# Optimization experiments

Measured on AMD Instinct MI355X. Metric: run time of the kernel, lower is better.

## Reference

```python
import jax, jax.numpy as jnp
import numpy as np

R = 8192        # rays
S_C = 64        # coarse samples per ray
S_F = 128       # fine samples per ray
NEAR, FAR = 2.0, 6.0
HIDDEN = 64
WHITE_BKGD = True
EPS_T = 1e-10   # transmittance eps (matches volumetric_rendering)
EPS_W = 1e-5    # weight-sum padding eps (matches piecewise_constant_pdf)


def setup_inputs() -> dict:
    key = jax.random.key(0)
    k0, k1, k2, k3, k4, k5 = jax.random.split(key, 6)
    return {
        "ray_origins": jax.random.normal(k0, (R, 3), jnp.float32),
        "ray_directions": jax.random.normal(k1, (R, 3), jnp.float32),
        "W1": jax.random.normal(k2, (6, HIDDEN), jnp.float32) * 0.5,
        "b1": jax.random.normal(k3, (HIDDEN,), jnp.float32) * 0.1,
        "W2": jax.random.normal(k4, (HIDDEN, 4), jnp.float32) * 0.3,
        "b2": jax.random.normal(k5, (4,), jnp.float32) * 0.1,
    }


def _mlp(coords, viewdirs, W1, b1, W2, b2):
    # coords: [R,S,3], viewdirs: [R,3] -> raw_rgb [R,S,3], raw_sigma [R,S]
    vd = jnp.broadcast_to(viewdirs[:, None, :], coords.shape)
    x = jnp.concatenate([coords, vd], axis=-1)            # [R,S,6]
    h = jax.nn.relu(jnp.einsum('rsi,ih->rsh', x, W1) + b1)
    out = jnp.einsum('rsh,ho->rso', h, W2) + b2           # [R,S,4]
    return out[..., :3], out[..., 3]


def _volrender(rgb, sigma, z_vals, directions):
    # rgb [R,S,3], sigma [R,S], z_vals [R,S], directions [R,3]
    dists = (z_vals[:, 1:] - z_vals[:, :-1]) * jnp.linalg.norm(directions, axis=-1, keepdims=True)
    alpha = 1.0 - jnp.exp(-sigma[:, :-1] * dists)         # [R,S-1]
    trans = jnp.concatenate([jnp.ones_like(alpha[:, :1]),
                             jnp.cumprod(1.0 - alpha + EPS_T, axis=-1)], axis=-1)
    alpha = jnp.concatenate([alpha, jnp.ones_like(alpha[:, :1])], axis=-1)
    weights = alpha * trans                               # [R,S]
    comp_rgb = jnp.einsum('rs,rsc->rc', weights, rgb)
    acc = weights.sum(-1)
    depth = (weights * z_vals).sum(-1)
    if WHITE_BKGD:
        comp_rgb = comp_rgb + (1.0 - acc)[:, None]
    return comp_rgb, weights, depth


def _piecewise_constant_pdf(bins, weights, num_samples):
    # bins [R,B+1], weights [R,B]; deterministic branch (randomized=False)
    nbins = weights.shape[-1]
    wsum = weights.sum(-1, keepdims=True)
    padding = jnp.maximum(0.0, EPS_W - wsum)
    weights = weights + padding / nbins
    wsum = wsum + padding
    pdf = weights / wsum
    cdf = jnp.minimum(1.0, jnp.cumsum(pdf[:, :-1], axis=-1))
    cdf = jnp.concatenate([jnp.zeros_like(cdf[:, :1]), cdf, jnp.ones_like(cdf[:, :1])], axis=-1)  # [R,B+1]
    u = jnp.linspace(0.0, 1.0 - jnp.finfo(jnp.float32).eps, num_samples)  # [F]
    mask = u[None, None, :] >= cdf[:, :, None]            # [R,B+1,F]

    def find_interval(x):  # x [R,B+1]
        x0 = jnp.max(jnp.where(mask, x[:, :, None], x[:, :1, None]), axis=1)
        x1 = jnp.min(jnp.where(~mask, x[:, :, None], x[:, -1:, None]), axis=1)
        return x0, x1

    bins_g0, bins_g1 = find_interval(bins)
    cdf_g0, cdf_g1 = find_interval(cdf)
    t = jnp.clip(jnp.nan_to_num((u[None, :] - cdf_g0) / (cdf_g1 - cdf_g0), nan=0.0), 0.0, 1.0)
    return jax.lax.stop_gradient(bins_g0 + t * (bins_g1 - bins_g0))  # [R,F]


def reference(ray_origins, ray_directions, W1, b1, W2, b2):
    Rn = ray_origins.shape[0]
    viewdirs = ray_directions / jnp.linalg.norm(ray_directions, axis=-1, keepdims=True)
    # coarse stratification (lindisp=False, randomized=False)
    t = jnp.linspace(0.0, 1.0, S_C)
    z_vals = jnp.broadcast_to(NEAR * (1.0 - t) + FAR * t, (Rn, S_C))
    coords = ray_origins[:, None, :] + z_vals[..., None] * ray_directions[:, None, :]
    raw_rgb, raw_sigma = _mlp(coords, viewdirs, W1, b1, W2, b2)
    rgb, sigma = jax.nn.sigmoid(raw_rgb), jax.nn.relu(raw_sigma)
    coarse_rgb, weights, coarse_depth = _volrender(rgb, sigma, z_vals, ray_directions)
    # hierarchical fine sampling via inverse-CDF over midpoint bins
    z_mid = 0.5 * (z_vals[:, 1:] + z_vals[:, :-1])
    z_samples = _piecewise_constant_pdf(z_mid, weights[:, 1:-1], S_F)
    z_fine = jnp.sort(jnp.concatenate([z_vals, z_samples], axis=-1), axis=-1)  # [R,S_C+S_F]
    coords = ray_origins[:, None, :] + z_fine[..., None] * ray_directions[:, None, :]
    # source falls through to coarse_model in the non-stateful branch; we mirror that (same MLP)
    raw_rgb, raw_sigma = _mlp(coords, viewdirs, W1, b1, W2, b2)
    rgb, sigma = jax.nn.sigmoid(raw_rgb), jax.nn.relu(raw_sigma)
    fine_rgb, _, fine_depth = _volrender(rgb, sigma, z_fine, ray_directions)
    return jnp.concatenate([coarse_rgb, coarse_depth[:, None], fine_rgb, fine_depth[:, None]], axis=-1)  # [R,8]
```

## Files before the change

kernel.cpp:

```cpp
#include <hip/hip_runtime.h>
#include <math.h>


#define RAYS   8192
#define NEARP  2.0f
#define FARP   6.0f
#define EPS_T  1e-10f
#define EPS_W  1e-5f
#define F32EPS 1.1920929e-7f

__device__ __forceinline__ float zc(int i) {
    const float t = (float)i * (1.0f / 63.0f);
    return NEARP * (1.0f - t) + FARP * t;
}
__device__ __forceinline__ float sigm(float x) { return 1.f / (1.f + __expf(-x)); }

__global__ __launch_bounds__(256) void nerf_kernel(
    const float* __restrict__ ro, const float* __restrict__ rd,
    const float* __restrict__ W1, const float* __restrict__ b1,
    const float* __restrict__ W2, const float* __restrict__ b2,
    float* __restrict__ out)
{
    __shared__ __align__(16) float sA[4][64];
    __shared__ __align__(16) float sB[4][64];
    __shared__ float sCdf[4][64];
    __shared__ float sZc [4][64];
    __shared__ float sZs [4][128];
    __shared__ float sZf [4][192];

    const int tid  = threadIdx.x;
    const int w    = tid >> 6;
    const int lane = tid & 63;
    const int ray  = blockIdx.x * 4 + w;

    const float ox = ro[ray * 3 + 0], oy = ro[ray * 3 + 1], oz = ro[ray * 3 + 2];
    const float dx = rd[ray * 3 + 0], dy = rd[ray * 3 + 1], dz = rd[ray * 3 + 2];
    const float norm = sqrtf(dx * dx + dy * dy + dz * dz);
    const float inv  = 1.f / norm;
    const float vx = dx * inv, vy = dy * inv, vz = dz * inv;

    {
        const float w10 = W1[lane],       w11 = W1[64 + lane],  w12 = W1[128 + lane];
        const float w13 = W1[192 + lane], w14 = W1[256 + lane], w15 = W1[320 + lane];
        float A = b1[lane];
        A = fmaf(vz, w15, A); A = fmaf(vy, w14, A); A = fmaf(vx, w13, A);
        A = fmaf(oz, w12, A); A = fmaf(oy, w11, A); A = fmaf(ox, w10, A);
        const float B = fmaf(dx, w10, fmaf(dy, w11, dz * w12));
        sA[w][lane] = A; sB[w][lane] = B;
    }
    __syncthreads();

    const float4* W2v = (const float4*)W2;
    const float bb0 = b2[0], bb1 = b2[1], bb2 = b2[2], bb3 = b2[3];

    const float z = zc(lane);
    sZc[w][lane] = z;
    float o0 = bb0, o1 = bb1, o2 = bb2, o3 = bb3;
#pragma unroll 4
    for (int i = 0; i < 16; ++i) {
        const float4 a4 = ((const float4*)sA[w])[i];
        const float4 b4 = ((const float4*)sB[w])[i];
        const float4 q0 = W2v[4 * i + 0], q1 = W2v[4 * i + 1];
        const float4 q2 = W2v[4 * i + 2], q3 = W2v[4 * i + 3];
        const float h0 = fmaxf(fmaf(z, b4.x, a4.x), 0.f);
        const float h1 = fmaxf(fmaf(z, b4.y, a4.y), 0.f);
        const float h2 = fmaxf(fmaf(z, b4.z, a4.z), 0.f);
        const float h3 = fmaxf(fmaf(z, b4.w, a4.w), 0.f);
        o0 = fmaf(h0, q0.x, o0); o1 = fmaf(h0, q0.y, o1); o2 = fmaf(h0, q0.z, o2); o3 = fmaf(h0, q0.w, o3);
        o0 = fmaf(h1, q1.x, o0); o1 = fmaf(h1, q1.y, o1); o2 = fmaf(h1, q1.z, o2); o3 = fmaf(h1, q1.w, o3);
        o0 = fmaf(h2, q2.x, o0); o1 = fmaf(h2, q2.y, o1); o2 = fmaf(h2, q2.z, o2); o3 = fmaf(h2, q2.w, o3);
        o0 = fmaf(h3, q3.x, o0); o1 = fmaf(h3, q3.y, o1); o2 = fmaf(h3, q3.z, o2); o3 = fmaf(h3, q3.w, o3);
    }
    const float r   = sigm(o0), g = sigm(o1), bl = sigm(o2);
    const float sig = fmaxf(o3, 0.f);

    const float znext = __shfl_down(z, 1);
    const float dist  = (znext - z) * norm;
    const float alpha = (lane < 63) ? (1.f - __expf(-sig * dist)) : 1.f;
    const float vfac  = 1.f - alpha + EPS_T;
    float p = vfac;
#pragma unroll
    for (int off = 1; off < 64; off <<= 1) {
        const float q = __shfl_up(p, off);
        if (lane >= off) p *= q;
    }
    float excl = __shfl_up(p, 1);
    if (lane == 0) excl = 1.f;
    const float wgt = alpha * excl;

    float sr = wgt * r, sg = wgt * g, sb = wgt * bl, sd = wgt * z;
#pragma unroll
    for (int m = 1; m < 64; m <<= 1) {
        sr += __shfl_xor(sr, m); sg += __shfl_xor(sg, m);
        sb += __shfl_xor(sb, m); sd += __shfl_xor(sd, m);
    }

    const float wmraw = __shfl_down(wgt, 1);
    const float wmv   = (lane < 62) ? wmraw : 0.f;
    float wsum = wmv;
#pragma unroll
    for (int m = 1; m < 64; m <<= 1) wsum += __shfl_xor(wsum, m);
    const float pad  = fmaxf(0.f, EPS_W - wsum);
    const float wadj = wmv + pad * (1.0f / 62.0f);
    const float wsp  = wsum + pad;
    const float pdf  = (lane < 62) ? (wadj / wsp) : 0.f;
    float ps = pdf;
#pragma unroll
    for (int off = 1; off < 64; off <<= 1) {
        const float q = __shfl_up(ps, off);
        if (lane >= off) ps += q;
    }
    if (lane < 61)  sCdf[w][lane + 1] = fminf(1.f, ps);
    if (lane == 61) sCdf[w][0]  = 0.f;
    if (lane == 62) sCdf[w][62] = 1.f;
    __syncthreads();

    float zsv[2];
#pragma unroll
    for (int j = 0; j < 2; ++j) {
        const int f = lane * 2 + j;
        const float u = (float)f * ((1.0f - F32EPS) / 127.0f);
        int lo = 0, hi = 62;
        while (hi - lo > 1) {
            const int mid = (lo + hi) >> 1;
            if (sCdf[w][mid] <= u) lo = mid; else hi = mid;
        }
        const float c0 = sCdf[w][lo], c1 = sCdf[w][lo + 1];
        const float den = c1 - c0;
        float tt = (den > 0.f) ? (u - c0) / den : 0.f;
        tt = fminf(fmaxf(tt, 0.f), 1.f);
        const float za = zc(lo), zb = zc(lo + 1), zd = zc(lo + 2);
        const float bin0 = 0.5f * (za + zb), bin1 = 0.5f * (zb + zd);
        const float zs = fmaf(tt, bin1 - bin0, bin0);
        zsv[j] = zs;
        sZs[w][f] = zs;
    }
    __syncthreads();

    {
        int lo = 0, hi = 128;
        while (lo < hi) { const int mid = (lo + hi) >> 1; if (sZs[w][mid] < z) lo = mid + 1; else hi = mid; }
        sZf[w][lane + lo] = z;
    }
#pragma unroll
    for (int j = 0; j < 2; ++j) {
        const float bv = zsv[j];
        const int f = lane * 2 + j;
        int lo = 0, hi = 64;
        while (lo < hi) { const int mid = (lo + hi) >> 1; if (sZc[w][mid] <= bv) lo = mid + 1; else hi = mid; }
        sZf[w][f + lo] = bv;
    }
    __syncthreads();

    const float zf0 = sZf[w][3 * lane + 0];
    const float zf1 = sZf[w][3 * lane + 1];
    const float zf2 = sZf[w][3 * lane + 2];
    const float zn2 = sZf[w][min(3 * lane + 3, 191)];

    float a0 = bb0, a1 = bb1, a2 = bb2, a3 = bb3;
    float e0 = bb0, e1 = bb1, e2 = bb2, e3 = bb3;
    float f0 = bb0, f1 = bb1, f2 = bb2, f3 = bb3;
#pragma unroll 2
    for (int i = 0; i < 16; ++i) {
        const float4 a4 = ((const float4*)sA[w])[i];
        const float4 b4 = ((const float4*)sB[w])[i];
        const float4 q0 = W2v[4 * i + 0], q1 = W2v[4 * i + 1];
        const float4 q2 = W2v[4 * i + 2], q3 = W2v[4 * i + 3];
        const float hA0 = fmaxf(fmaf(zf0, b4.x, a4.x), 0.f);
        const float hA1 = fmaxf(fmaf(zf0, b4.y, a4.y), 0.f);
        const float hA2 = fmaxf(fmaf(zf0, b4.z, a4.z), 0.f);
        const float hA3 = fmaxf(fmaf(zf0, b4.w, a4.w), 0.f);
        const float hB0 = fmaxf(fmaf(zf1, b4.x, a4.x), 0.f);
        const float hB1 = fmaxf(fmaf(zf1, b4.y, a4.y), 0.f);
        const float hB2 = fmaxf(fmaf(zf1, b4.z, a4.z), 0.f);
        const float hB3 = fmaxf(fmaf(zf1, b4.w, a4.w), 0.f);
        const float hC0 = fmaxf(fmaf(zf2, b4.x, a4.x), 0.f);
        const float hC1 = fmaxf(fmaf(zf2, b4.y, a4.y), 0.f);
        const float hC2 = fmaxf(fmaf(zf2, b4.z, a4.z), 0.f);
        const float hC3 = fmaxf(fmaf(zf2, b4.w, a4.w), 0.f);
        a0 = fmaf(hA0, q0.x, a0); a1 = fmaf(hA0, q0.y, a1); a2 = fmaf(hA0, q0.z, a2); a3 = fmaf(hA0, q0.w, a3);
        a0 = fmaf(hA1, q1.x, a0); a1 = fmaf(hA1, q1.y, a1); a2 = fmaf(hA1, q1.z, a2); a3 = fmaf(hA1, q1.w, a3);
        a0 = fmaf(hA2, q2.x, a0); a1 = fmaf(hA2, q2.y, a1); a2 = fmaf(hA2, q2.z, a2); a3 = fmaf(hA2, q2.w, a3);
        a0 = fmaf(hA3, q3.x, a0); a1 = fmaf(hA3, q3.y, a1); a2 = fmaf(hA3, q3.z, a2); a3 = fmaf(hA3, q3.w, a3);
        e0 = fmaf(hB0, q0.x, e0); e1 = fmaf(hB0, q0.y, e1); e2 = fmaf(hB0, q0.z, e2); e3 = fmaf(hB0, q0.w, e3);
        e0 = fmaf(hB1, q1.x, e0); e1 = fmaf(hB1, q1.y, e1); e2 = fmaf(hB1, q1.z, e2); e3 = fmaf(hB1, q1.w, e3);
        e0 = fmaf(hB2, q2.x, e0); e1 = fmaf(hB2, q2.y, e1); e2 = fmaf(hB2, q2.z, e2); e3 = fmaf(hB2, q2.w, e3);
        e0 = fmaf(hB3, q3.x, e0); e1 = fmaf(hB3, q3.y, e1); e2 = fmaf(hB3, q3.z, e2); e3 = fmaf(hB3, q3.w, e3);
        f0 = fmaf(hC0, q0.x, f0); f1 = fmaf(hC0, q0.y, f1); f2 = fmaf(hC0, q0.z, f2); f3 = fmaf(hC0, q0.w, f3);
        f0 = fmaf(hC1, q1.x, f0); f1 = fmaf(hC1, q1.y, f1); f2 = fmaf(hC1, q1.z, f2); f3 = fmaf(hC1, q1.w, f3);
        f0 = fmaf(hC2, q2.x, f0); f1 = fmaf(hC2, q2.y, f1); f2 = fmaf(hC2, q2.z, f2); f3 = fmaf(hC2, q2.w, f3);
        f0 = fmaf(hC3, q3.x, f0); f1 = fmaf(hC3, q3.y, f1); f2 = fmaf(hC3, q3.z, f2); f3 = fmaf(hC3, q3.w, f3);
    }
    const float r0s = sigm(a0), g0s = sigm(a1), b0s = sigm(a2), s0 = fmaxf(a3, 0.f);
    const float r1s = sigm(e0), g1s = sigm(e1), b1s = sigm(e2), s1 = fmaxf(e3, 0.f);
    const float r2s = sigm(f0), g2s = sigm(f1), b2s = sigm(f2), s2 = fmaxf(f3, 0.f);

    const float d0 = (zf1 - zf0) * norm, d1 = (zf2 - zf1) * norm, d2 = (zn2 - zf2) * norm;
    const float al0 = 1.f - __expf(-s0 * d0);
    const float al1 = 1.f - __expf(-s1 * d1);
    const float al2 = (lane < 63) ? (1.f - __expf(-s2 * d2)) : 1.f;
    const float v0 = 1.f - al0 + EPS_T, v1 = 1.f - al1 + EPS_T, v2 = 1.f - al2 + EPS_T;

    float lp = v0 * v1 * v2;
#pragma unroll
    for (int off = 1; off < 64; off <<= 1) {
        const float q = __shfl_up(lp, off);
        if (lane >= off) lp *= q;
    }
    float ex = __shfl_up(lp, 1);
    if (lane == 0) ex = 1.f;
    const float tr1 = ex * v0, tr2 = tr1 * v1;
    const float w0 = al0 * ex, w1 = al1 * tr1, w2 = al2 * tr2;

    float fr = fmaf(w0, r0s, fmaf(w1, r1s, w2 * r2s));
    float fg = fmaf(w0, g0s, fmaf(w1, g1s, w2 * g2s));
    float fb = fmaf(w0, b0s, fmaf(w1, b1s, w2 * b2s));
    float fd = fmaf(w0, zf0, fmaf(w1, zf1, w2 * zf2));
#pragma unroll
    for (int m = 1; m < 64; m <<= 1) {
        fr += __shfl_xor(fr, m); fg += __shfl_xor(fg, m);
        fb += __shfl_xor(fb, m); fd += __shfl_xor(fd, m);
    }

    if (lane == 0) {
        float* po = out + (size_t)ray * 8;
        po[0] = sr; po[1] = sg; po[2] = sb; po[3] = sd;
        po[4] = fr; po[5] = fg; po[6] = fb; po[7] = fd;
    }
}

extern "C" void kernel_launch(void* const* d_in, const int* in_sizes, int n_in,
                              void* d_out, int out_size, void* d_ws, size_t ws_size,
                              hipStream_t stream) {
    const float* ro = (const float*)d_in[0];
    const float* rd = (const float*)d_in[1];
    const float* W1 = (const float*)d_in[2];
    const float* b1 = (const float*)d_in[3];
    const float* W2 = (const float*)d_in[4];
    const float* b2 = (const float*)d_in[5];
    float* out = (float*)d_out;
    nerf_kernel<<<dim3(RAYS / 4), dim3(256), 0, stream>>>(ro, rd, W1, b1, W2, b2, out);
}
```

Baseline: 90.26 us.

## Use packed float2 FMA for MLP and move per-ray A/B to global workspace

Rewrites both MLP loops using two-wide vector FMA/max builtins so the compiler can emit packed FP32 instructions (v_pk_fma_f32), aiming to halve VALU instruction count in the dominant compute. It also moves the per-ray first-layer A/B vectors from shared memory into a global workspace buffer, replacing the block barrier with a block-scope fence. The fence plus cross-lane global reads is a weaker guarantee than the barrier, and global loads replace LDS reads, which may add latency or cause correctness issues if visibility is not ensured.

```diff
diff --git a/kernel.cpp b/kernel.cpp
--- a/kernel.cpp
+++ b/kernel.cpp
@@ -9,6 +9,11 @@
 #define EPS_W  1e-5f
 #define F32EPS 1.1920929e-7f
 
+typedef float v2f __attribute__((ext_vector_type(2)));
+__device__ __forceinline__ v2f mk2(float a, float b) { v2f r; r.x = a; r.y = b; return r; }
+__device__ __forceinline__ v2f pfma(v2f a, v2f b, v2f c) { return __builtin_elementwise_fma(a, b, c); }
+__device__ __forceinline__ v2f pmax0(v2f a) { return __builtin_elementwise_max(a, mk2(0.f, 0.f)); }
+
 __device__ __forceinline__ float zc(int i) {
     const float t = (float)i * (1.0f / 63.0f);
     return NEARP * (1.0f - t) + FARP * t;
@@ -19,10 +24,8 @@
     const float* __restrict__ ro, const float* __restrict__ rd,
     const float* __restrict__ W1, const float* __restrict__ b1,
     const float* __restrict__ W2, const float* __restrict__ b2,
-    float* __restrict__ out)
+    float* __restrict__ out, float* __restrict__ ws)
 {
-    __shared__ __align__(16) float sA[4][64];
-    __shared__ __align__(16) float sB[4][64];
     __shared__ float sCdf[4][64];
     __shared__ float sZc [4][64];
     __shared__ float sZs [4][128];
@@ -39,6 +42,7 @@
     const float inv  = 1.f / norm;
     const float vx = dx * inv, vy = dy * inv, vz = dz * inv;
 
+    float* wsray = ws + (size_t)ray * 128;
     {
         const float w10 = W1[lane],       w11 = W1[64 + lane],  w12 = W1[128 + lane];
         const float w13 = W1[192 + lane], w14 = W1[256 + lane], w15 = W1[320 + lane];
@@ -46,33 +50,38 @@
         A = fmaf(vz, w15, A); A = fmaf(vy, w14, A); A = fmaf(vx, w13, A);
         A = fmaf(oz, w12, A); A = fmaf(oy, w11, A); A = fmaf(ox, w10, A);
         const float B = fmaf(dx, w10, fmaf(dy, w11, dz * w12));
-        sA[w][lane] = A; sB[w][lane] = B;
-    }
-    __syncthreads();
+        wsray[lane] = A; wsray[64 + lane] = B;
+    }
+    __threadfence_block();
+    const float4* ABa = (const float4*)wsray;
+    const float4* ABb = (const float4*)(wsray + 64);
 
     const float4* W2v = (const float4*)W2;
     const float bb0 = b2[0], bb1 = b2[1], bb2 = b2[2], bb3 = b2[3];
 
     const float z = zc(lane);
     sZc[w][lane] = z;
-    float o0 = bb0, o1 = bb1, o2 = bb2, o3 = bb3;
+    const v2f zz = mk2(z, z);
+    v2f o01 = mk2(bb0, bb1), o23 = mk2(bb2, bb3);
 #pragma unroll 4
     for (int i = 0; i < 16; ++i) {
-        const float4 a4 = ((const float4*)sA[w])[i];
-        const float4 b4 = ((const float4*)sB[w])[i];
+        const float4 a4 = ABa[i];
+        const float4 b4 = ABb[i];
         const float4 q0 = W2v[4 * i + 0], q1 = W2v[4 * i + 1];
         const float4 q2 = W2v[4 * i + 2], q3 = W2v[4 * i + 3];
-        const float h0 = fmaxf(fmaf(z, b4.x, a4.x), 0.f);
-        const float h1 = fmaxf(fmaf(z, b4.y, a4.y), 0.f);
-        const float h2 = fmaxf(fmaf(z, b4.z, a4.z), 0.f);
-        const float h3 = fmaxf(fmaf(z, b4.w, a4.w), 0.f);
-        o0 = fmaf(h0, q0.x, o0); o1 = fmaf(h0, q0.y, o1); o2 = fmaf(h0, q0.z, o2); o3 = fmaf(h0, q0.w, o3);
-        o0 = fmaf(h1, q1.x, o0); o1 = fmaf(h1, q1.y, o1); o2 = fmaf(h1, q1.z, o2); o3 = fmaf(h1, q1.w, o3);
-        o0 = fmaf(h2, q2.x, o0); o1 = fmaf(h2, q2.y, o1); o2 = fmaf(h2, q2.z, o2); o3 = fmaf(h2, q2.w, o3);
-        o0 = fmaf(h3, q3.x, o0); o1 = fmaf(h3, q3.y, o1); o2 = fmaf(h3, q3.z, o2); o3 = fmaf(h3, q3.w, o3);
-    }
-    const float r   = sigm(o0), g = sigm(o1), bl = sigm(o2);
-    const float sig = fmaxf(o3, 0.f);
+        const v2f hL = pmax0(pfma(zz, mk2(b4.x, b4.y), mk2(a4.x, a4.y)));
+        const v2f hH = pmax0(pfma(zz, mk2(b4.z, b4.w), mk2(a4.z, a4.w)));
+        o01 = pfma(mk2(hL.x, hL.x), mk2(q0.x, q0.y), o01);
+        o23 = pfma(mk2(hL.x, hL.x), mk2(q0.z, q0.w), o23);
+        o01 = pfma(mk2(hL.y, hL.y), mk2(q1.x, q1.y), o01);
+        o23 = pfma(mk2(hL.y, hL.y), mk2(q1.z, q1.w), o23);
+        o01 = pfma(mk2(hH.x, hH.x), mk2(q2.x, q2.y), o01);
+        o23 = pfma(mk2(hH.x, hH.x), mk2(q2.z, q2.w), o23);
+        o01 = pfma(mk2(hH.y, hH.y), mk2(q3.x, q3.y), o01);
+        o23 = pfma(mk2(hH.y, hH.y), mk2(q3.z, q3.w), o23);
+    }
+    const float r   = sigm(o01.x), g = sigm(o01.y), bl = sigm(o23.x);
+    const float sig = fmaxf(o23.y, 0.f);
 
     const float znext = __shfl_down(z, 1);
     const float dist  = (znext - z) * norm;
@@ -157,43 +166,41 @@
     const float zf2 = sZf[w][3 * lane + 2];
     const float zn2 = sZf[w][min(3 * lane + 3, 191)];
 
-    float a0 = bb0, a1 = bb1, a2 = bb2, a3 = bb3;
-    float e0 = bb0, e1 = bb1, e2 = bb2, e3 = bb3;
-    float f0 = bb0, f1 = bb1, f2 = bb2, f3 = bb3;
+    const v2f zA = mk2(zf0, zf0), zB = mk2(zf1, zf1), zC = mk2(zf2, zf2);
+    v2f a01 = mk2(bb0, bb1), a23 = mk2(bb2, bb3);
+    v2f e01 = mk2(bb0, bb1), e23 = mk2(bb2, bb3);
+    v2f f01 = mk2(bb0, bb1), f23 = mk2(bb2, bb3);
 #pragma unroll 2
     for (int i = 0; i < 16; ++i) {
-        const float4 a4 = ((const float4*)sA[w])[i];
-        const float4 b4 = ((const float4*)sB[w])[i];
+        const float4 a4 = ABa[i];
+        const float4 b4 = ABb[i];
         const float4 q0 = W2v[4 * i + 0], q1 = W2v[4 * i + 1];
         const float4 q2 = W2v[4 * i + 2], q3 = W2v[4 * i + 3];
-        const float hA0 = fmaxf(fmaf(zf0, b4.x, a4.x), 0.f);
-        const float hA1 = fmaxf(fmaf(zf0, b4.y, a4.y), 0.f);
-        const float hA2 = fmaxf(fmaf(zf0, b4.z, a4.z), 0.f);
-        const float hA3 = fmaxf(fmaf(zf0, b4.w, a4.w), 0.f);
-        const float hB0 = fmaxf(fmaf(zf1, b4.x, a4.x), 0.f);
-        const float hB1 = fmaxf(fmaf(zf1, b4.y, a4.y), 0.f);
-        const float hB2 = fmaxf(fmaf(zf1, b4.z, a4.z), 0.f);
-        const float hB3 = fmaxf(fmaf(zf1, b4.w, a4.w), 0.f);
-        const float hC0 = fmaxf(fmaf(zf2, b4.x, a4.x), 0.f);
-        const float hC1 = fmaxf(fmaf(zf2, b4.y, a4.y), 0.f);
-        const float hC2 = fmaxf(fmaf(zf2, b4.z, a4.z), 0.f);
-        const float hC3 = fmaxf(fmaf(zf2, b4.w, a4.w), 0.f);
-        a0 = fmaf(hA0, q0.x, a0); a1 = fmaf(hA0, q0.y, a1); a2 = fmaf(hA0, q0.z, a2); a3 = fmaf(hA0, q0.w, a3);
-        a0 = fmaf(hA1, q1.x, a0); a1 = fmaf(hA1, q1.y, a1); a2 = fmaf(hA1, q1.z, a2); a3 = fmaf(hA1, q1.w, a3);
-        a0 = fmaf(hA2, q2.x, a0); a1 = fmaf(hA2, q2.y, a1); a2 = fmaf(hA2, q2.z, a2); a3 = fmaf(hA2, q2.w, a3);
-        a0 = fmaf(hA3, q3.x, a0); a1 = fmaf(hA3, q3.y, a1); a2 = fmaf(hA3, q3.z, a2); a3 = fmaf(hA3, q3.w, a3);
-        e0 = fmaf(hB0, q0.x, e0); e1 = fmaf(hB0, q0.y, e1); e2 = fmaf(hB0, q0.z, e2); e3 = fmaf(hB0, q0.w, e3);
-        e0 = fmaf(hB1, q1.x, e0); e1 = fmaf(hB1, q1.y, e1); e2 = fmaf(hB1, q1.z, e2); e3 = fmaf(hB1, q1.w, e3);
-        e0 = fmaf(hB2, q2.x, e0); e1 = fmaf(hB2, q2.y, e1); e2 = fmaf(hB2, q2.z, e2); e3 = fmaf(hB2, q2.w, e3);
-        e0 = fmaf(hB3, q3.x, e0); e1 = fmaf(hB3, q3.y, e1); e2 = fmaf(hB3, q3.z, e2); e3 = fmaf(hB3, q3.w, e3);
-        f0 = fmaf(hC0, q0.x, f0); f1 = fmaf(hC0, q0.y, f1); f2 = fmaf(hC0, q0.z, f2); f3 = fmaf(hC0, q0.w, f3);
-        f0 = fmaf(hC1, q1.x, f0); f1 = fmaf(hC1, q1.y, f1); f2 = fmaf(hC1, q1.z, f2); f3 = fmaf(hC1, q1.w, f3);
-        f0 = fmaf(hC2, q2.x, f0); f1 = fmaf(hC2, q2.y, f1); f2 = fmaf(hC2, q2.z, f2); f3 = fmaf(hC2, q2.w, f3);
-        f0 = fmaf(hC3, q3.x, f0); f1 = fmaf(hC3, q3.y, f1); f2 = fmaf(hC3, q3.z, f2); f3 = fmaf(hC3, q3.w, f3);
-    }
-    const float r0s = sigm(a0), g0s = sigm(a1), b0s = sigm(a2), s0 = fmaxf(a3, 0.f);
-    const float r1s = sigm(e0), g1s = sigm(e1), b1s = sigm(e2), s1 = fmaxf(e3, 0.f);
-    const float r2s = sigm(f0), g2s = sigm(f1), b2s = sigm(f2), s2 = fmaxf(f3, 0.f);
+        const v2f blo = mk2(b4.x, b4.y), bhi = mk2(b4.z, b4.w);
+        const v2f alo = mk2(a4.x, a4.y), ahi = mk2(a4.z, a4.w);
+        const v2f hAL = pmax0(pfma(zA, blo, alo)), hAH = pmax0(pfma(zA, bhi, ahi));
+        const v2f hBL = pmax0(pfma(zB, blo, alo)), hBH = pmax0(pfma(zB, bhi, ahi));
+        const v2f hCL = pmax0(pfma(zC, blo, alo)), hCH = pmax0(pfma(zC, bhi, ahi));
+        const v2f q0a = mk2(q0.x, q0.y), q0b = mk2(q0.z, q0.w);
+        const v2f q1a = mk2(q1.x, q1.y), q1b = mk2(q1.z, q1.w);
+        const v2f q2a = mk2(q2.x, q2.y), q2b = mk2(q2.z, q2.w);
+        const v2f q3a = mk2(q3.x, q3.y), q3b = mk2(q3.z, q3.w);
+        a01 = pfma(mk2(hAL.x, hAL.x), q0a, a01); a23 = pfma(mk2(hAL.x, hAL.x), q0b, a23);
+        a01 = pfma(mk2(hAL.y, hAL.y), q1a, a01); a23 = pfma(mk2(hAL.y, hAL.y), q1b, a23);
+        a01 = pfma(mk2(hAH.x, hAH.x), q2a, a01); a23 = pfma(mk2(hAH.x, hAH.x), q2b, a23);
+        a01 = pfma(mk2(hAH.y, hAH.y), q3a, a01); a23 = pfma(mk2(hAH.y, hAH.y), q3b, a23);
+        e01 = pfma(mk2(hBL.x, hBL.x), q0a, e01); e23 = pfma(mk2(hBL.x, hBL.x), q0b, e23);
+        e01 = pfma(mk2(hBL.y, hBL.y), q1a, e01); e23 = pfma(mk2(hBL.y, hBL.y), q1b, e23);
+        e01 = pfma(mk2(hBH.x, hBH.x), q2a, e01); e23 = pfma(mk2(hBH.x, hBH.x), q2b, e23);
+        e01 = pfma(mk2(hBH.y, hBH.y), q3a, e01); e23 = pfma(mk2(hBH.y, hBH.y), q3b, e23);
+        f01 = pfma(mk2(hCL.x, hCL.x), q0a, f01); f23 = pfma(mk2(hCL.x, hCL.x), q0b, f23);
+        f01 = pfma(mk2(hCL.y, hCL.y), q1a, f01); f23 = pfma(mk2(hCL.y, hCL.y), q1b, f23);
+        f01 = pfma(mk2(hCH.x, hCH.x), q2a, f01); f23 = pfma(mk2(hCH.x, hCH.x), q2b, f23);
+        f01 = pfma(mk2(hCH.y, hCH.y), q3a, f01); f23 = pfma(mk2(hCH.y, hCH.y), q3b, f23);
+    }
+    const float r0s = sigm(a01.x), g0s = sigm(a01.y), b0s = sigm(a23.x), s0 = fmaxf(a23.y, 0.f);
+    const float r1s = sigm(e01.x), g1s = sigm(e01.y), b1s = sigm(e23.x), s1 = fmaxf(e23.y, 0.f);
+    const float r2s = sigm(f01.x), g2s = sigm(f01.y), b2s = sigm(f23.x), s2 = fmaxf(f23.y, 0.f);
 
     const float d0 = (zf1 - zf0) * norm, d1 = (zf2 - zf1) * norm, d2 = (zn2 - zf2) * norm;
     const float al0 = 1.f - __expf(-s0 * d0);
@@ -239,5 +246,6 @@
     const float* W2 = (const float*)d_in[4];
     const float* b2 = (const float*)d_in[5];
     float* out = (float*)d_out;
-    nerf_kernel<<<dim3(RAYS / 4), dim3(256), 0, stream>>>(ro, rd, W1, b1, W2, b2, out);
+    float* ws  = (float*)d_ws;
+    nerf_kernel<<<dim3(RAYS / 4), dim3(256), 0, stream>>>(ro, rd, W1, b1, W2, b2, out, ws);
 }
```

New measurement: 90.90 us. Within noise of the previous version (+0.7%).
